# Kernel optimization log

Measured on AMD Instinct MI355X. Metric: run time of the kernel, lower is better.

## Reference

```python
import jax, jax.numpy as jnp
import numpy as np

DIM = 1024          # dim_feature
NUM_CLUSTERS = 8
N_PER = 4096        # patches per cluster (equal-size clusters)
NUM_SAMPLE = 1024   # num_sample_feature
QDIM = 128          # q projection dim
# sample_ratio = NUM_SAMPLE / (NUM_CLUSTERS*N_PER) = 1/32 -> top_k per cluster
TOPK = int(np.rint(N_PER * NUM_SAMPLE / (NUM_CLUSTERS * N_PER)))  # 128


def setup_inputs() -> dict:
    key = jax.random.key(0)
    ks = jax.random.split(key, 6)
    s = 1.0 / np.sqrt(DIM)
    return {
        "cluster_features": jax.random.normal(ks[0], (NUM_CLUSTERS, N_PER, DIM), jnp.float32),
        "key_feats": jax.random.normal(ks[1], (NUM_CLUSTERS, 1, DIM), jnp.float32),
        "q_w": jax.random.normal(ks[2], (QDIM, DIM), jnp.float32) * s,
        "q_b": jax.random.normal(ks[3], (QDIM,), jnp.float32) * 0.01,
        "v_w": jax.random.normal(ks[4], (DIM, DIM), jnp.float32) * s,
        "v_b": jax.random.normal(ks[5], (DIM,), jnp.float32) * 0.01,
    }


def reference(cluster_features, key_feats, q_w, q_b, v_w, v_b):
    scale_q = jnp.sqrt(jnp.float32(QDIM))

    def per_cluster(feats, key_feat):
        # NonLocalRanking with top_k=TOPK, top_fuse=False (adaptive path)
        Q = feats @ q_w.T + q_b            # [N, 128]
        qk = key_feat @ q_w.T + q_b        # [1, 128]
        A = (Q @ qk.T) / scale_q           # [N, 1]
        A = jax.nn.softmax(A, axis=0)      # softmax over patches (dim 0)
        _, idx = jax.lax.top_k(A[:, 0], TOPK)
        top_feats = feats[idx]             # [TOPK, DIM]
        V = feats @ v_w.T + v_b            # [N, DIM]
        fusion = (A.T @ V)[0]              # [DIM]
        return top_feats, fusion

    tops, fus = jax.vmap(per_cluster)(cluster_features, key_feats)
    selected = tops.reshape(-1, DIM)       # [NUM_CLUSTERS*TOPK, DIM] == [NUM_SAMPLE, DIM]
    # module pads/truncates to NUM_SAMPLE; here it is exactly NUM_SAMPLE
    selected = selected[:NUM_SAMPLE]
    return selected, fus
```

## Files before the change

### kernel.cpp

```cpp
#include <hip/hip_runtime.h>
#include <math.h>


#define DIM   1024
#define NC    8
#define NPER  4096
#define QD    128
#define TOPK  128
#define K1B   128
#define JS    16

typedef unsigned long long u64;
typedef __attribute__((ext_vector_type(2))) unsigned long long ull2;
typedef __attribute__((ext_vector_type(4))) float f4;

__global__ __launch_bounds__(256) void k0_prep(
    const float* __restrict__ key_feats, const float* __restrict__ q_w,
    const float* __restrict__ q_b, float* __restrict__ w_all)
{
    const int c  = blockIdx.x >> 2, jc = blockIdx.x & 3;
    const int tid = threadIdx.x;
    __shared__ float part[256];
    __shared__ float qs[QD];

    {
        const int k = tid >> 1, half = tid & 1;
        const float4* qr4 = (const float4*)(q_w + (size_t)k * DIM + half * 512);
        const float4* kf4 = (const float4*)(key_feats + (size_t)c * DIM + half * 512);
        float s = 0.f;
        #pragma unroll 16
        for (int j = 0; j < 128; ++j) {
            float4 a = qr4[j], b = kf4[j];
            s += a.x*b.x + a.y*b.y + a.z*b.z + a.w*b.w;
        }
        part[tid] = s;
    }
    __syncthreads();
    if (tid < QD) qs[tid] = part[2*tid] + part[2*tid+1] + q_b[tid];
    __syncthreads();

    const int j = jc * 256 + tid;
    float s = 0.f;
    #pragma unroll 16
    for (int k = 0; k < QD; ++k)
        s += q_w[(size_t)k * DIM + j] * qs[k];
    w_all[c * DIM + j] = s * 0.08838834764831845f;
}

__global__ __launch_bounds__(256, 4) void k1_main(
    const float* __restrict__ feats, const float* __restrict__ w_all,
    u64* __restrict__ keys,
    float* __restrict__ pacc,
    float* __restrict__ pm, float* __restrict__ pz)
{
    const int c    = blockIdx.y;
    const int blk  = blockIdx.x;
    const int tid  = threadIdx.x;
    const int lane = tid & 63;
    const int wave = tid >> 6;

    const float4* w4 = (const float4*)(w_all + c * DIM);
    float4 wv[4];
    #pragma unroll
    for (int q = 0; q < 4; ++q) wv[q] = w4[lane + 64*q];

    float4 acc[4];
    #pragma unroll
    for (int q = 0; q < 4; ++q) acc[q] = make_float4(0.f, 0.f, 0.f, 0.f);
    float m = -INFINITY, Z = 0.f;

    const int wslot = blk * 4 + wave;
    const float* fc = feats + (size_t)c * NPER * DIM;

    f4 fA[4], fB[4];
    {
        const f4* f4p = (const f4*)(fc + (size_t)wslot * DIM);
        #pragma unroll
        for (int q = 0; q < 4; ++q) fA[q] = __builtin_nontemporal_load(f4p + lane + 64*q);
    }

    #define K1_PROCESS(FREG, ROW)                                              \
    do {                                                                       \
        float p = 0.f;                                                         \
        _Pragma("unroll")                                                      \
        for (int q = 0; q < 4; ++q)                                            \
            p += FREG[q].x*wv[q].x + FREG[q].y*wv[q].y +                       \
                 FREG[q].z*wv[q].z + FREG[q].w*wv[q].w;                        \
        _Pragma("unroll")                                                      \
        for (int off = 32; off > 0; off >>= 1) p += __shfl_xor(p, off, 64);    \
        if (lane == 0) {                                                       \
            unsigned int b = __float_as_uint(p);                               \
            unsigned int u = b ^ ((b & 0x80000000u) ? 0xFFFFFFFFu : 0x80000000u); \
            keys[c * NPER + (ROW)] = ((u64)u << 32) | (unsigned int)(~(ROW));  \
        }                                                                      \
        if (p > m) {                  \
            const float sOld = __expf(m - p);                                  \
            Z = Z * sOld + 1.f;                                                \
            _Pragma("unroll")                                                  \
            for (int q = 0; q < 4; ++q) {                                      \
                acc[q].x = acc[q].x * sOld + FREG[q].x;                        \
                acc[q].y = acc[q].y * sOld + FREG[q].y;                        \
                acc[q].z = acc[q].z * sOld + FREG[q].z;                        \
                acc[q].w = acc[q].w * sOld + FREG[q].w;                        \
            }                                                                  \
            m = p;                                                             \
        } else {                                                               \
            const float t = __expf(p - m);                                     \
            Z += t;                                                            \
            _Pragma("unroll")                                                  \
            for (int q = 0; q < 4; ++q) {                                      \
                acc[q].x += t * FREG[q].x;                                     \
                acc[q].y += t * FREG[q].y;                                     \
                acc[q].z += t * FREG[q].z;                                     \
                acc[q].w += t * FREG[q].w;                                     \
            }                                                                  \
        }                                                                      \
    } while (0)

    for (int it = 0; it < 8; it += 2) {
        const int r0 = wslot + 512 * it;
        {
            const f4* f4p = (const f4*)(fc + (size_t)(r0 + 512) * DIM);
            #pragma unroll
            for (int q = 0; q < 4; ++q) fB[q] = __builtin_nontemporal_load(f4p + lane + 64*q);
        }
        K1_PROCESS(fA, r0);
        if (it + 2 < 8) {
            const f4* f4p = (const f4*)(fc + (size_t)(r0 + 1024) * DIM);
            #pragma unroll
            for (int q = 0; q < 4; ++q) fA[q] = __builtin_nontemporal_load(f4p + lane + 64*q);
        }
        K1_PROCESS(fB, r0 + 512);
    }
    #undef K1_PROCESS

    __shared__ float sm[4], sz[4];
    __shared__ float sacc[4][DIM];
    if (lane == 0) { sm[wave] = m; sz[wave] = Z; }
    #pragma unroll
    for (int q = 0; q < 4; ++q)
        ((float4*)sacc[wave])[lane + 64*q] = acc[q];
    __syncthreads();

    const float mb = fmaxf(fmaxf(sm[0], sm[1]), fmaxf(sm[2], sm[3]));
    const float e0 = __expf(sm[0] - mb), e1 = __expf(sm[1] - mb);
    const float e2 = __expf(sm[2] - mb), e3 = __expf(sm[3] - mb);
    float4 a0 = ((float4*)sacc[0])[tid];
    float4 a1 = ((float4*)sacc[1])[tid];
    float4 a2 = ((float4*)sacc[2])[tid];
    float4 a3 = ((float4*)sacc[3])[tid];
    float4 o;
    o.x = a0.x*e0 + a1.x*e1 + a2.x*e2 + a3.x*e3;
    o.y = a0.y*e0 + a1.y*e1 + a2.y*e2 + a3.y*e3;
    o.z = a0.z*e0 + a1.z*e1 + a2.z*e2 + a3.z*e3;
    o.w = a0.w*e0 + a1.w*e1 + a2.w*e2 + a3.w*e3;
    ((float4*)(pacc + (size_t)(c * K1B + blk) * DIM))[tid] = o;
    if (tid == 0) {
        pm[c * K1B + blk] = mb;
        pz[c * K1B + blk] = sz[0]*e0 + sz[1]*e1 + sz[2]*e2 + sz[3]*e3;
    }
}

__global__ __launch_bounds__(256) void fat_a(
    const float* __restrict__ pacc, const float* __restrict__ pm,
    const float* __restrict__ pz, float* __restrict__ g,
    const u64* __restrict__ keys, int* __restrict__ part)
{
    const int tid = threadIdx.x;
    if (blockIdx.x < 32) {
        const int c = blockIdx.x >> 2, jb = blockIdx.x & 3;
        const int slot = tid & 63;
        const int bg   = tid >> 6;
        __shared__ float spm[K1B], spz[K1B], swe[K1B];
        __shared__ float szc;
        __shared__ float4 sred[3][64];

        if (tid < K1B) spm[tid] = pm[c*K1B + tid];
        else spz[tid - K1B] = pz[c*K1B + tid - K1B];
        __syncthreads();
        float mc = -INFINITY;
        for (int b = 0; b < K1B; ++b) mc = fmaxf(mc, spm[b]);
        if (tid < K1B) swe[tid] = __expf(spm[tid] - mc);
        __syncthreads();
        if (tid == 0) {
            float z = 0.f;
            for (int b = 0; b < K1B; ++b) z += spz[b] * swe[b];
            szc = z;
        }

        const int jbase = jb * 256 + slot * 4;
        float4 a = make_float4(0.f, 0.f, 0.f, 0.f);
        #pragma unroll
        for (int k = 0; k < 32; ++k) {
            const int b = bg * 32 + k;
            const float e = swe[b];
            float4 v = *(const float4*)(pacc + (size_t)(c*K1B + b) * DIM + jbase);
            a.x += e*v.x; a.y += e*v.y; a.z += e*v.z; a.w += e*v.w;
        }
        if (bg) sred[bg-1][slot] = a;
        __syncthreads();
        if (bg == 0) {
            float4 t0 = sred[0][slot], t1 = sred[1][slot], t2 = sred[2][slot];
            const float inv = 1.0f / szc;
            float4 o;
            o.x = (a.x + t0.x + t1.x + t2.x) * inv;
            o.y = (a.y + t0.y + t1.y + t2.y) * inv;
            o.z = (a.z + t0.z + t1.z + t2.z) * inv;
            o.w = (a.w + t0.w + t1.w + t2.w) * inv;
            *(float4*)(g + c * DIM + jbase) = o;
        }
    } else {
        const int t = blockIdx.x - 32;
        const int iblk = t & 3, js = (t >> 2) & (JS-1), c = t >> 6;
        __shared__ u64 lk[256];
        if (tid < 128)
            ((float4*)lk)[tid] = ((const float4*)(keys + c * NPER + js * 256))[tid];

        const int ibase = iblk * 1024;
        u64 ki[4];
        #pragma unroll
        for (int q = 0; q < 4; ++q) ki[q] = keys[c * NPER + ibase + tid + 256*q];
        __syncthreads();

        int cnt0 = 0, cnt1 = 0, cnt2 = 0, cnt3 = 0;
        const ull2* lk2 = (const ull2*)lk;
        #pragma unroll 4
        for (int jt = 0; jt < 128; ++jt) {
            ull2 kj = lk2[jt];
            cnt0 += (kj.x > ki[0]) + (kj.y > ki[0]);
            cnt1 += (kj.x > ki[1]) + (kj.y > ki[1]);
            cnt2 += (kj.x > ki[2]) + (kj.y > ki[2]);
            cnt3 += (kj.x > ki[3]) + (kj.y > ki[3]);
        }
        int* dst = part + ((js * NC + c) << 12) + ibase + tid;
        dst[0]   = cnt0; dst[256] = cnt1; dst[512] = cnt2; dst[768] = cnt3;
    }
}

__global__ __launch_bounds__(256) void fat_b(
    const int* __restrict__ part, const float* __restrict__ feats,
    float* __restrict__ out_sel,
    const float* __restrict__ v_w, const float* __restrict__ v_b,
    const float* __restrict__ g, float* __restrict__ fus)
{
    const int tid = threadIdx.x;
    if (blockIdx.x < 128) {
        const int c = blockIdx.x >> 4;
        const int i = (blockIdx.x & 15) * 256 + tid;
        __shared__ int list_i[TOPK], list_r[TOPK];
        __shared__ int cnt;
        if (tid == 0) cnt = 0;
        __syncthreads();

        int r = 0;
        #pragma unroll
        for (int js = 0; js < JS; ++js) r += part[((js * NC + c) << 12) + i];
        if (r < TOPK) {
            const int s = atomicAdd(&cnt, 1);
            list_i[s] = i; list_r[s] = r;
        }
        __syncthreads();

        const int n = cnt;
        if (n > 0) {
            const float* fc = feats + (size_t)c * NPER * DIM;
            float4 cur = ((const float4*)(fc + (size_t)list_i[0] * DIM))[tid];
            for (int s = 0; s < n; ++s) {
                float4 nxt;
                if (s + 1 < n)
                    nxt = ((const float4*)(fc + (size_t)list_i[s+1] * DIM))[tid];
                ((float4*)(out_sel + ((size_t)c * TOPK + list_r[s]) * DIM))[tid] = cur;
                cur = nxt;
            }
        }
    } else {
        __shared__ float4 sg[NC][256];
        const int lane = tid & 63, wave = tid >> 6;
        for (int t = tid; t < NC * 256; t += 256)
            ((float4*)sg)[t] = ((const float4*)g)[t];
        __syncthreads();

        const int row0 = (blockIdx.x - 128) * 8 + wave * 2;
        for (int rr = 0; rr < 2; ++rr) {
            const int o = row0 + rr;
            const float4* vr = (const float4*)(v_w + (size_t)o * DIM);
            float4 v[4];
            #pragma unroll
            for (int u = 0; u < 4; ++u) v[u] = vr[lane + 64*u];
            float p[NC];
            #pragma unroll
            for (int cc = 0; cc < NC; ++cc) {
                float s = 0.f;
                #pragma unroll
                for (int u = 0; u < 4; ++u) {
                    float4 gv = sg[cc][lane + 64*u];
                    s += v[u].x*gv.x + v[u].y*gv.y + v[u].z*gv.z + v[u].w*gv.w;
                }
                p[cc] = s;
            }
            #pragma unroll
            for (int off = 32; off > 0; off >>= 1) {
                #pragma unroll
                for (int cc = 0; cc < NC; ++cc) p[cc] += __shfl_xor(p[cc], off, 64);
            }
            if (lane == 0) {
                const float b = v_b[o];
                #pragma unroll
                for (int cc = 0; cc < NC; ++cc) fus[cc * DIM + o] = p[cc] + b;
            }
        }
    }
}

extern "C" void kernel_launch(void* const* d_in, const int* in_sizes, int n_in,
                              void* d_out, int out_size, void* d_ws, size_t ws_size,
                              hipStream_t stream) {
    const float* feats     = (const float*)d_in[0];
    const float* key_feats = (const float*)d_in[1];
    const float* q_w       = (const float*)d_in[2];
    const float* q_b       = (const float*)d_in[3];
    const float* v_w       = (const float*)d_in[4];
    const float* v_b       = (const float*)d_in[5];
    float* out      = (float*)d_out;
    float* out_sel  = out;
    float* out_fus  = out + (size_t)1024 * 1024;

    u64*   keys   = (u64*)d_ws;
    float* pacc   = (float*)(keys + NC * NPER);
    float* pm     = pacc + (size_t)NC * K1B * DIM;
    float* pz     = pm + NC * K1B;
    float* g      = pz + NC * K1B;
    float* w_all  = g + NC * DIM;
    int*   part   = (int*)(w_all + NC * DIM);

    k0_prep <<<dim3(NC * 4),       256, 0, stream>>>(key_feats, q_w, q_b, w_all);
    k1_main <<<dim3(K1B, NC),      256, 0, stream>>>(feats, w_all, keys, pacc, pm, pz);
    fat_a   <<<dim3(32 + 4*JS*NC), 256, 0, stream>>>(pacc, pm, pz, g, keys, part);
    fat_b   <<<dim3(256),          256, 0, stream>>>(part, feats, out_sel, v_w, v_b, g, out_fus);
}
```

Baseline: 241.4 us.

## Replace all-pairs top-k ranking with histogram radix-select plus candidate ranking

The top-k selection no longer counts rank against all 4096 keys across 512 blocks. It now runs one block per cluster that builds a 4096-bin histogram on the top 12 key bits, finds the bin containing the k-th key, collects the candidates in or above that bin and ranks only those against each other. Each block writes the selected indices directly, so the gather kernel reads 128 indices per cluster instead of summing 16 partial counts for every patch. The gather also uses nontemporal loads and stores. The risk is that a heavily populated critical bin makes the M² candidate loop slow, and the stage now has only 8 blocks, which is far less parallelism.

```diff
diff --git a/kernel.cpp b/kernel.cpp
--- a/kernel.cpp
+++ b/kernel.cpp
@@ -8,7 +8,6 @@
 #define QD    128
 #define TOPK  128
 #define K1B   128
-#define JS    16
 
 typedef unsigned long long u64;
 typedef __attribute__((ext_vector_type(2))) unsigned long long ull2;
@@ -164,7 +163,7 @@
 __global__ __launch_bounds__(256) void fat_a(
     const float* __restrict__ pacc, const float* __restrict__ pm,
     const float* __restrict__ pz, float* __restrict__ g,
-    const u64* __restrict__ keys, int* __restrict__ part)
+    const u64* __restrict__ keys, int* __restrict__ selIdx)
 {
     const int tid = threadIdx.x;
     if (blockIdx.x < 32) {
@@ -210,68 +209,96 @@
             *(float4*)(g + c * DIM + jbase) = o;
         }
     } else {
-        const int t = blockIdx.x - 32;
-        const int iblk = t & 3, js = (t >> 2) & (JS-1), c = t >> 6;
-        __shared__ u64 lk[256];
-        if (tid < 128)
-            ((float4*)lk)[tid] = ((const float4*)(keys + c * NPER + js * 256))[tid];
-
-        const int ibase = iblk * 1024;
-        u64 ki[4];
-        #pragma unroll
-        for (int q = 0; q < 4; ++q) ki[q] = keys[c * NPER + ibase + tid + 256*q];
-        __syncthreads();
-
-        int cnt0 = 0, cnt1 = 0, cnt2 = 0, cnt3 = 0;
-        const ull2* lk2 = (const ull2*)lk;
-        #pragma unroll 4
-        for (int jt = 0; jt < 128; ++jt) {
-            ull2 kj = lk2[jt];
-            cnt0 += (kj.x > ki[0]) + (kj.y > ki[0]);
-            cnt1 += (kj.x > ki[1]) + (kj.y > ki[1]);
-            cnt2 += (kj.x > ki[2]) + (kj.y > ki[2]);
-            cnt3 += (kj.x > ki[3]) + (kj.y > ki[3]);
-        }
-        int* dst = part + ((js * NC + c) << 12) + ibase + tid;
-        dst[0]   = cnt0; dst[256] = cnt1; dst[512] = cnt2; dst[768] = cnt3;
+        const int c = blockIdx.x - 32;
+        __shared__ u64 lk[NPER];
+        __shared__ int hist[4096];
+        __shared__ unsigned short cand[NPER];
+        __shared__ int chunkSuf[256];
+        __shared__ int critBin, candCnt;
+
+        for (int t = tid; t < NPER/2; t += 256)
+            ((ull2*)lk)[t] = ((const ull2*)(keys + (size_t)c * NPER))[t];
+        for (int t = tid; t < 4096; t += 256) hist[t] = 0;
+        if (tid == 0) candCnt = 0;
+        __syncthreads();
+
+        #pragma unroll
+        for (int q = 0; q < 16; ++q)
+            atomicAdd(&hist[(int)(lk[tid + 256*q] >> 52)], 1);
+        __syncthreads();
+
+        {
+            int s = 0;
+            #pragma unroll
+            for (int b = 0; b < 16; ++b) s += hist[tid*16 + b];
+            chunkSuf[tid] = s;
+        }
+        __syncthreads();
+        if (tid == 0) {
+            int run = 0;
+            for (int t = 255; t >= 0; --t) {
+                const int v = chunkSuf[t]; chunkSuf[t] = run; run += v;
+            }
+        }
+        __syncthreads();
+        {
+            int run = chunkSuf[tid];
+            for (int b = 15; b >= 0; --b) {
+                const int bin = tid*16 + b;
+                const int h = hist[bin];
+                if (run < TOPK && run + h >= TOPK) critBin = bin;
+                run += h;
+            }
+        }
+        __syncthreads();
+        const int B = critBin;
+
+        #pragma unroll
+        for (int q = 0; q < 16; ++q) {
+            const int i = tid + 256*q;
+            if ((int)(lk[i] >> 52) >= B) {
+                const int s = atomicAdd(&candCnt, 1);
+                cand[s] = (unsigned short)i;
+            }
+        }
+        __syncthreads();
+
+        const int M = candCnt;
+        for (int s = tid; s < M; s += 256) {
+            const int i = (int)cand[s];
+            const u64 ki = lk[i];
+            int r = 0;
+            for (int j = 0; j < M; ++j)
+                r += (lk[(int)cand[j]] > ki) ? 1 : 0;
+            if (r < TOPK) selIdx[c * TOPK + r] = i;
+        }
     }
 }
 
 __global__ __launch_bounds__(256) void fat_b(
-    const int* __restrict__ part, const float* __restrict__ feats,
+    const int* __restrict__ selIdx, const float* __restrict__ feats,
     float* __restrict__ out_sel,
     const float* __restrict__ v_w, const float* __restrict__ v_b,
     const float* __restrict__ g, float* __restrict__ fus)
 {
     const int tid = threadIdx.x;
     if (blockIdx.x < 128) {
-        const int c = blockIdx.x >> 4;
-        const int i = (blockIdx.x & 15) * 256 + tid;
-        __shared__ int list_i[TOPK], list_r[TOPK];
-        __shared__ int cnt;
-        if (tid == 0) cnt = 0;
-        __syncthreads();
-
-        int r = 0;
-        #pragma unroll
-        for (int js = 0; js < JS; ++js) r += part[((js * NC + c) << 12) + i];
-        if (r < TOPK) {
-            const int s = atomicAdd(&cnt, 1);
-            list_i[s] = i; list_r[s] = r;
-        }
-        __syncthreads();
-
-        const int n = cnt;
-        if (n > 0) {
-            const float* fc = feats + (size_t)c * NPER * DIM;
-            float4 cur = ((const float4*)(fc + (size_t)list_i[0] * DIM))[tid];
-            for (int s = 0; s < n; ++s) {
-                float4 nxt;
-                if (s + 1 < n)
-                    nxt = ((const float4*)(fc + (size_t)list_i[s+1] * DIM))[tid];
-                ((float4*)(out_sel + ((size_t)c * TOPK + list_r[s]) * DIM))[tid] = cur;
-                cur = nxt;
-            }
+        const int c  = blockIdx.x >> 4;
+        const int r0 = (blockIdx.x & 15) * 8;
+        const float* fc = feats + (size_t)c * NPER * DIM;
+        const int* sic = selIdx + c * TOPK + r0;
+
+        f4 cur = __builtin_nontemporal_load(
+            (const f4*)(fc + (size_t)sic[0] * DIM) + tid);
+        #pragma unroll
+        for (int s = 0; s < 8; ++s) {
+            f4 nxt;
+            if (s + 1 < 8)
+                nxt = __builtin_nontemporal_load(
+                    (const f4*)(fc + (size_t)sic[s+1] * DIM) + tid);
+            __builtin_nontemporal_store(
+                cur, (f4*)(out_sel + ((size_t)c * TOPK + r0 + s) * DIM) + tid);
+            if (s + 1 < 8) cur = nxt;
         }
     } else {
         __shared__ float4 sg[NC][256];
@@ -331,10 +358,10 @@
     float* pz     = pm + NC * K1B;
     float* g      = pz + NC * K1B;
     float* w_all  = g + NC * DIM;
-    int*   part   = (int*)(w_all + NC * DIM);
-
-    k0_prep <<<dim3(NC * 4),       256, 0, stream>>>(key_feats, q_w, q_b, w_all);
-    k1_main <<<dim3(K1B, NC),      256, 0, stream>>>(feats, w_all, keys, pacc, pm, pz);
-    fat_a   <<<dim3(32 + 4*JS*NC), 256, 0, stream>>>(pacc, pm, pz, g, keys, part);
-    fat_b   <<<dim3(256),          256, 0, stream>>>(part, feats, out_sel, v_w, v_b, g, out_fus);
-}
+    int*   selIdx = (int*)(w_all + NC * DIM);
+
+    k0_prep <<<dim3(NC * 4),  256, 0, stream>>>(key_feats, q_w, q_b, w_all);
+    k1_main <<<dim3(K1B, NC), 256, 0, stream>>>(feats, w_all, keys, pacc, pm, pz);
+    fat_a   <<<dim3(32 + NC), 256, 0, stream>>>(pacc, pm, pz, g, keys, selIdx);
+    fat_b   <<<dim3(256),     256, 0, stream>>>(selIdx, feats, out_sel, v_w, v_b, g, out_fus);
+}
```

Measured after the change: 235.7 us. 2.4% less time.
